# Kernel tuning notes

Measured on AMD Instinct MI355X. Metric: run time of the kernel, lower is better.

The kernel has to match this reference:

```python
import jax, jax.numpy as jnp
import numpy as np

N = 131072   # n_agents
K = 2        # k_neighbors = k_obstacles
H, C = 4, 128
HC = H * C   # 512
OBS_DIM = 37
OUT = 4


def setup_inputs() -> dict:
    key = jax.random.key(0)
    ks = jax.random.split(key, 40)
    s = 0.05
    def g(i, shape):
        return jax.random.normal(ks[i], shape, dtype=jnp.float32) * s
    inp = {"obs": jax.random.normal(ks[0], (N, OBS_DIM), dtype=jnp.float32)}
    # layer 0 (query_dim = 19)
    inp["wq0"] = g(1, (19, HC)); inp["wak0"] = g(2, (6, HC)); inp["wav0"] = g(3, (7, HC))
    inp["wok0"] = g(4, (2, HC)); inp["wov0"] = g(5, (2, HC))
    inp["apw0"] = g(6, (HC, C)); inp["apb0"] = jnp.zeros((C,), jnp.float32)
    inp["opw0"] = g(7, (HC, C)); inp["opb0"] = jnp.zeros((C,), jnp.float32)
    inp["fpw0"] = g(8, (2 * C, C)); inp["fpb0"] = jnp.zeros((C,), jnp.float32)
    inp["ca0"] = jnp.float32(1.0); inp["co0"] = jnp.float32(2.0)
    # layer 1 (query_dim = gnn_hidden_dim = 128)
    inp["wq1"] = g(9, (C, HC)); inp["wak1"] = g(10, (6, HC)); inp["wav1"] = g(11, (7, HC))
    inp["wok1"] = g(12, (2, HC)); inp["wov1"] = g(13, (2, HC))
    inp["apw1"] = g(14, (HC, C)); inp["apb1"] = jnp.zeros((C,), jnp.float32)
    inp["opw1"] = g(15, (HC, C)); inp["opb1"] = jnp.zeros((C,), jnp.float32)
    inp["fpw1"] = g(16, (2 * C, C)); inp["fpb1"] = jnp.zeros((C,), jnp.float32)
    inp["ca1"] = jnp.float32(1.0); inp["co1"] = jnp.float32(2.0)
    # output head
    inp["headw"] = g(17, (C, OUT)); inp["headb"] = jnp.zeros((OUT,), jnp.float32)
    return inp


def _forward(obs, wq0, wak0, wav0, wok0, wov0, apw0, apb0, opw0, opb0, fpw0, fpb0, ca0, co0,
             wq1, wak1, wav1, wok1, wov1, apw1, apb1, opw1, opb1, fpw1, fpb1, ca1, co1,
             headw, headb):
    n = obs.shape[0]
    scale = (C // H) ** -0.5  # matches torch: (out_channels // heads) ** -0.5

    # feature extraction per ObservationConfig (k=2)
    qf = jnp.concatenate([obs[:, 0:12], obs[:, 30:37]], axis=-1)        # [n, 19]
    nb = obs[:, 12:24].reshape(n, K, 6)                                  # neighbor keys [n,k,6]
    nbv = jnp.concatenate([nb, obs[:, 24:26][..., None]], axis=-1)       # + progress -> [n,k,7]
    ob = obs[:, 26:30].reshape(n, K, 2)                                  # obstacle k/v [n,k,2]
    apos = obs[:, 0:2]
    npos = nb[..., 0:2]
    opos = ob

    def attend(q, kfeat, vfeat, wk, wv, pw, pb, decay, pos_k):
        keys = (kfeat @ wk).reshape(n, K, H, C)
        vals = (vfeat @ wv).reshape(n, K, H, C)
        dist = jnp.linalg.norm(apos[:, None, :] - pos_k, axis=-1)        # [n,k]
        dw = jnp.exp(-decay * dist)                                      # [n,k]
        dot = jnp.einsum('nhc,nkhc->nhk', q, keys) * scale
        att = jax.nn.softmax(dot * dw[:, None, :], axis=-1)
        out = jnp.einsum('nhk,nkhc->nhc', att, vals).reshape(n, HC)
        return out @ pw + pb                                             # [n, C]

    def layer(qfeat, wq, wak, wav, wok, wov, apw, apb, opw, opb, fpw, fpb, ca, co):
        q = (qfeat @ wq).reshape(n, H, C)
        a = attend(q, nb, nbv, wak, wav, apw, apb, ca, npos)
        o = attend(q, ob, ob, wok, wov, opw, opb, co, opos)
        return jnp.concatenate([a, o], axis=-1) @ fpw + fpb              # [n, C]

    h = layer(qf, wq0, wak0, wav0, wok0, wov0, apw0, apb0, opw0, opb0, fpw0, fpb0, ca0, co0)
    h = layer(h, wq1, wak1, wav1, wok1, wov1, apw1, apb1, opw1, opb1, fpw1, fpb1, ca1, co1)
    return h @ headw + headb                                             # [n, OUT]


def reference(obs, wq0, wak0, wav0, wok0, wov0, apw0, apb0, opw0, opb0, fpw0, fpb0, ca0, co0,
              wq1, wak1, wav1, wok1, wov1, apw1, apb1, opw1, opb1, fpw1, fpb1, ca1, co1,
              headw, headb):
    return _forward(obs, wq0, wak0, wav0, wok0, wov0, apw0, apb0, opw0, opb0, fpw0, fpb0, ca0, co0,
                    wq1, wak1, wav1, wok1, wov1, apw1, apb1, opw1, opb1, fpw1, fpb1, ca1, co1,
                    headw, headb)
```

## Files before the change

### kernel.cpp

```cpp
#include <hip/hip_runtime.h>
#include <math.h>

#define NTH 256

typedef float v4f __attribute__((ext_vector_type(4)));

enum : int {
  WQ0_OFF = 0,
  M_OFF   = 608,
  TB_OFF  = 1760,
  AO1_OFF = 1792,
  B1H_OFF = 1936,
  PA0_OFF  = 2048,
  PO0_OFF  = 5632,
  PA1_OFF  = 6656,
  PO1_OFF  = 10240,
  WQ1T_OFF = 11264,
  B0_OFF   = 15360,
  BB1_OFF  = 15488,
  HWT_OFF  = 15616,
  WS_END   = 16128
};

__global__ __launch_bounds__(NTH) void prepA(
    const float* __restrict__ wq0,  const float* __restrict__ wak0, const float* __restrict__ wok0,
    const float* __restrict__ wav0, const float* __restrict__ wov0,
    const float* __restrict__ apw0, const float* __restrict__ opw0,
    const float* __restrict__ wq1,  const float* __restrict__ wak1, const float* __restrict__ wok1,
    const float* __restrict__ wav1, const float* __restrict__ wov1,
    const float* __restrict__ apw1, const float* __restrict__ opw1,
    const float* __restrict__ fpw0, const float* __restrict__ fpw1,
    const float* __restrict__ fpb0, const float* __restrict__ apb0, const float* __restrict__ opb0,
    const float* __restrict__ fpb1, const float* __restrict__ apb1, const float* __restrict__ opb1,
    const float* __restrict__ headw, float* __restrict__ ws)
{
  const int b = blockIdx.x;
  const int tid = threadIdx.x;
  const float scale = 0.17677669529663687f;

  if (b < 9) {
    const int idx = b * NTH + tid;
    const float* w; const v4f* p4; int t4, outv;
    if (idx < 896) {
      int h = idx / 224, r = idx % 224, i = r >> 5; t4 = r & 31;
      w = wav0 + i * 512 + h * 128; p4 = (const v4f*)(apw0 + h * 16384);
      outv = (PA0_OFF >> 2) + (h * 7 + i) * 32 + t4;
    } else if (idx < 1152) {
      int k = idx - 896; int h = k >> 6, i = (k >> 5) & 1; t4 = k & 31;
      w = wov0 + i * 512 + h * 128; p4 = (const v4f*)(opw0 + h * 16384);
      outv = (PO0_OFF >> 2) + (h * 2 + i) * 32 + t4;
    } else if (idx < 2048) {
      int k = idx - 1152; int h = k / 224, r = k % 224, i = r >> 5; t4 = r & 31;
      w = wav1 + i * 512 + h * 128; p4 = (const v4f*)(apw1 + h * 16384);
      outv = (PA1_OFF >> 2) + (h * 7 + i) * 32 + t4;
    } else {
      int k = idx - 2048; int h = k >> 6, i = (k >> 5) & 1; t4 = k & 31;
      w = wov1 + i * 512 + h * 128; p4 = (const v4f*)(opw1 + h * 16384);
      outv = (PO1_OFF >> 2) + (h * 2 + i) * 32 + t4;
    }
    v4f acc = (v4f)0.f;
#pragma unroll 32
    for (int c = 0; c < 128; ++c) acc += w[c] * p4[c * 32 + t4];
    ((v4f*)ws)[outv] = acc;
  } else if (b < 25) {
    const int idx = (b - 9) * NTH + tid;
    const int cc = idx & 127, j = (idx >> 7) & 7, h = idx >> 10;
    const v4f* a4 = (const v4f*)(wq1 + cc * 512 + h * 128);
    const v4f* b4 = (const v4f*)(((j < 6) ? wak1 + j * 512 : wok1 + (j - 6) * 512) + h * 128);
    v4f s = (v4f)0.f;
#pragma unroll 16
    for (int c4 = 0; c4 < 32; ++c4) s += a4[c4] * b4[c4];
    ws[WQ1T_OFF + (h * 8 + j) * 128 + cc] = s[0] + s[1] + s[2] + s[3];
  } else if (b < 28) {
    const int idx = (b - 25) * NTH + tid;
    if (idx < 608) {
      const int j = idx & 7, r = (idx >> 3) % 19, h = idx / 152;
      const v4f* a4 = (const v4f*)(wq0 + r * 512 + h * 128);
      const v4f* b4 = (const v4f*)(((j < 6) ? wak0 + j * 512 : wok0 + (j - 6) * 512) + h * 128);
      v4f s = (v4f)0.f;
#pragma unroll 16
      for (int c4 = 0; c4 < 32; ++c4) s += a4[c4] * b4[c4];
      ws[WQ0_OFF + idx] = (s[0] + s[1] + s[2] + s[3]) * scale;
    }
  } else if (b == 28) {
    __shared__ v4f red[256];
    const int isB1 = tid >> 7;
    const int s = tid & 127, j4 = s & 31, g = s >> 5;
    const v4f* fp4 = (const v4f*)(isB1 ? fpw1 : fpw0);
    const float* ab = isB1 ? apb1 : apb0;
    const float* ob = isB1 ? opb1 : opb0;
    const v4f* fb4 = (const v4f*)(isB1 ? fpb1 : fpb0);
    v4f acc = (v4f)0.f;
#pragma unroll 32
    for (int c = g * 32; c < g * 32 + 32; ++c)
      acc += ab[c] * fp4[c * 32 + j4] + ob[c] * fp4[(128 + c) * 32 + j4];
    red[tid] = acc;
    __syncthreads();
    if (g == 0) {
      v4f r = red[tid] + red[tid + 32] + red[tid + 64] + red[tid + 96] + fb4[j4];
      ((v4f*)(ws + (isB1 ? BB1_OFF : B0_OFF)))[j4] = r;
    }
  } else {
    for (int e = tid; e < 512; e += NTH) {
      const int o = e >> 7, c = e & 127;
      ws[HWT_OFF + e] = headw[c * 4 + o];
    }
  }
}

__global__ __launch_bounds__(NTH) void prepB(
    const float* __restrict__ fpw0, const float* __restrict__ fpw1,
    const float* __restrict__ headb, float* __restrict__ ws)
{
  const int b = blockIdx.x;
  const int tid = threadIdx.x;
  const float scale = 0.17677669529663687f;
  __shared__ v4f sred[256];
  __shared__ float sV[128];

  if (b < 72) {
    const int isL1 = (b >= 36) ? 1 : 0;
    const int t = isL1 ? b - 36 : b;
    const int h = t / 9, i = t % 9;
    const int x4 = tid & 31, g = tid >> 5;
    const float* P = ws + (i < 7
        ? (isL1 ? PA1_OFF : PA0_OFF) + (h * 7 + i) * 128
        : (isL1 ? PO1_OFF : PO0_OFF) + (h * 2 + (i - 7)) * 128);
    const v4f* f4 = (const v4f*)((isL1 ? fpw1 : fpw0) + (i < 7 ? 0 : 16384));
    v4f acc = (v4f)0.f;
#pragma unroll
    for (int u = g * 16; u < g * 16 + 16; ++u) acc += P[u] * f4[u * 32 + x4];
    sred[tid] = acc;
    __syncthreads();
    if (g == 0) {
      v4f r = sred[x4];
#pragma unroll
      for (int q = 1; q < 8; ++q) r += sred[q * 32 + x4];
      ((v4f*)sV)[x4] = r;
    }
    __syncthreads();
    if (!isL1) {
      if (tid < 32) {
        const int h2 = tid >> 3, j2 = tid & 7;
        const v4f* W4 = (const v4f*)(ws + WQ1T_OFF + (h2 * 8 + j2) * 128);
        const v4f* A4 = (const v4f*)sV;
        v4f a = (v4f)0.f;
#pragma unroll
        for (int c4 = 0; c4 < 32; ++c4) a += A4[c4] * W4[c4];
        ws[M_OFF + t * 32 + tid] = (a[0] + a[1] + a[2] + a[3]) * scale;
      }
    } else {
      if (tid < 4) {
        const v4f* H4 = (const v4f*)(ws + HWT_OFF + tid * 128);
        const v4f* R4 = (const v4f*)sV;
        v4f a = (v4f)0.f;
#pragma unroll
        for (int c4 = 0; c4 < 32; ++c4) a += R4[c4] * H4[c4];
        ws[AO1_OFF + t * 4 + tid] = a[0] + a[1] + a[2] + a[3];
      }
    }
  } else {
    if (tid < 32) {
      const int h = tid >> 3, j = tid & 7;
      const v4f* B4 = (const v4f*)(ws + B0_OFF);
      const v4f* W4 = (const v4f*)(ws + WQ1T_OFF + (h * 8 + j) * 128);
      v4f a = (v4f)0.f;
#pragma unroll
      for (int c4 = 0; c4 < 32; ++c4) a += B4[c4] * W4[c4];
      ws[TB_OFF + tid] = (a[0] + a[1] + a[2] + a[3]) * scale;
    } else if (tid < 36) {
      const int o = tid - 32;
      const v4f* B4 = (const v4f*)(ws + BB1_OFF);
      const v4f* H4 = (const v4f*)(ws + HWT_OFF + o * 128);
      v4f a = (v4f)0.f;
#pragma unroll
      for (int c4 = 0; c4 < 32; ++c4) a += B4[c4] * H4[c4];
      ws[B1H_OFF + o] = a[0] + a[1] + a[2] + a[3] + headb[o];
    }
  }
}

__global__ __launch_bounds__(NTH) void actor_main(
    const float* __restrict__ obs, const float* __restrict__ ws,
    const float* __restrict__ pca0, const float* __restrict__ pco0,
    const float* __restrict__ pca1, const float* __restrict__ pco1,
    float* __restrict__ out, int n)
{
  const int tid = threadIdx.x;
  const int gid = blockIdx.x * NTH + tid;

  __shared__ v4f sObsV[NTH * 37 / 4];
  float* sObs = (float*)sObsV;
  {
    const size_t total_f = (size_t)n * 37;
    const size_t v4base = (size_t)blockIdx.x * (NTH * 37 / 4);
    const v4f* src = (const v4f*)obs;
#pragma unroll
    for (int k = 0; k < 9; k++) {
      const size_t vi = v4base + k * NTH + tid;
      if (vi * 4 + 4 <= total_f) {
        sObsV[k * NTH + tid] = src[vi];
      } else {
#pragma unroll
        for (int e = 0; e < 4; e++) {
          const size_t f = vi * 4 + e;
          if (f < total_f) sObs[(k * NTH + tid) * 4 + e] = obs[f];
        }
      }
    }
    if (tid < 64) {
      const size_t vi = v4base + 9 * NTH + tid;
      if (vi * 4 + 4 <= total_f) {
        sObsV[9 * NTH + tid] = src[vi];
      } else {
#pragma unroll
        for (int e = 0; e < 4; e++) {
          const size_t f = vi * 4 + e;
          if (f < total_f) sObs[(9 * NTH + tid) * 4 + e] = obs[f];
        }
      }
    }
  }
  __syncthreads();
  if (gid >= n) return;

  const v4f* __restrict__ tbl = (const v4f*)ws;

  float o[37];
#pragma unroll
  for (int i = 0; i < 37; i++) o[i] = sObs[tid * 37 + i];

  float qf[19];
#pragma unroll
  for (int i = 0; i < 12; i++) qf[i] = o[i];
#pragma unroll
  for (int i = 0; i < 7; i++) qf[12 + i] = o[30 + i];
  float nb[2][6];
#pragma unroll
  for (int k2 = 0; k2 < 2; k2++)
#pragma unroll
    for (int i = 0; i < 6; i++) nb[k2][i] = o[12 + 6 * k2 + i];
  const float nbv6[2] = { o[24], o[25] };
  const float obf[2][2] = { { o[26], o[27] }, { o[28], o[29] } };
  const float ax = o[0], ay = o[1];

  float dista[2], disto[2];
#pragma unroll
  for (int k2 = 0; k2 < 2; k2++) {
    float dx = ax - nb[k2][0], dy = ay - nb[k2][1];
    dista[k2] = sqrtf(dx * dx + dy * dy);
    float ex = ax - obf[k2][0], ey = ay - obf[k2][1];
    disto[k2] = sqrtf(ex * ex + ey * ey);
  }
  const float ca0 = pca0[0], co0 = pco0[0], ca1 = pca1[0], co1 = pco1[0];
  float dwa0[2], dwo0[2], dwa1[2], dwo1[2];
#pragma unroll
  for (int k2 = 0; k2 < 2; k2++) {
    dwa0[k2] = __expf(-ca0 * dista[k2]);
    dwo0[k2] = __expf(-co0 * disto[k2]);
    dwa1[k2] = __expf(-ca1 * dista[k2]);
    dwo1[k2] = __expf(-co1 * disto[k2]);
  }

  v4f t0v[8];
#pragma unroll
  for (int z = 0; z < 8; z++) t0v[z] = (v4f)0.f;
#pragma unroll
  for (int h = 0; h < 4; h++) {
#pragma unroll
    for (int r = 0; r < 19; r++) {
      float q = qf[r];
      t0v[h * 2 + 0] += tbl[(h * 19 + r) * 2 + 0] * q;
      t0v[h * 2 + 1] += tbl[(h * 19 + r) * 2 + 1] * q;
    }
  }

  float wff[36];
#pragma unroll
  for (int h = 0; h < 4; h++) {
    float la[2], lo[2];
#pragma unroll
    for (int k2 = 0; k2 < 2; k2++) {
      float da = t0v[h*2][0]*nb[k2][0] + t0v[h*2][1]*nb[k2][1] + t0v[h*2][2]*nb[k2][2]
               + t0v[h*2][3]*nb[k2][3] + t0v[h*2+1][0]*nb[k2][4] + t0v[h*2+1][1]*nb[k2][5];
      la[k2] = da * dwa0[k2];
      float dof = t0v[h*2+1][2]*obf[k2][0] + t0v[h*2+1][3]*obf[k2][1];
      lo[k2] = dof * dwo0[k2];
    }
    float e  = __expf(la[1] - la[0]); float aa1 = e  / (1.f + e);  float aa0 = 1.f - aa1;
    float eo = __expf(lo[1] - lo[0]); float bo1 = eo / (1.f + eo); float bo0 = 1.f - bo1;
#pragma unroll
    for (int i = 0; i < 6; i++) wff[h * 9 + i] = aa0 * nb[0][i] + aa1 * nb[1][i];
    wff[h * 9 + 6] = aa0 * nbv6[0] + aa1 * nbv6[1];
    wff[h * 9 + 7] = bo0 * obf[0][0] + bo1 * obf[1][0];
    wff[h * 9 + 8] = bo0 * obf[0][1] + bo1 * obf[1][1];
  }

  v4f t1v[8];
#pragma unroll
  for (int q = 0; q < 8; q++) t1v[q] = tbl[440 + q];
#pragma unroll
  for (int t = 0; t < 36; t++) {
    float f = wff[t];
#pragma unroll
    for (int q = 0; q < 8; q++)
      t1v[q] += tbl[152 + t * 8 + q] * f;
  }

  float wf1f[36];
#pragma unroll
  for (int h = 0; h < 4; h++) {
    float la[2], lo[2];
#pragma unroll
    for (int k2 = 0; k2 < 2; k2++) {
      float da = t1v[h*2][0]*nb[k2][0] + t1v[h*2][1]*nb[k2][1] + t1v[h*2][2]*nb[k2][2]
               + t1v[h*2][3]*nb[k2][3] + t1v[h*2+1][0]*nb[k2][4] + t1v[h*2+1][1]*nb[k2][5];
      la[k2] = da * dwa1[k2];
      float dof = t1v[h*2+1][2]*obf[k2][0] + t1v[h*2+1][3]*obf[k2][1];
      lo[k2] = dof * dwo1[k2];
    }
    float e  = __expf(la[1] - la[0]); float aa1 = e  / (1.f + e);  float aa0 = 1.f - aa1;
    float eo = __expf(lo[1] - lo[0]); float bo1 = eo / (1.f + eo); float bo0 = 1.f - bo1;
#pragma unroll
    for (int i = 0; i < 6; i++) wf1f[h * 9 + i] = aa0 * nb[0][i] + aa1 * nb[1][i];
    wf1f[h * 9 + 6] = aa0 * nbv6[0] + aa1 * nbv6[1];
    wf1f[h * 9 + 7] = bo0 * obf[0][0] + bo1 * obf[1][0];
    wf1f[h * 9 + 8] = bo0 * obf[0][1] + bo1 * obf[1][1];
  }

  v4f acc = tbl[484];
#pragma unroll
  for (int t = 0; t < 36; t++)
    acc += tbl[448 + t] * wf1f[t];
  ((v4f*)out)[gid] = acc;
}

extern "C" void kernel_launch(void* const* d_in, const int* in_sizes, int n_in,
                              void* d_out, int out_size, void* d_ws, size_t ws_size,
                              hipStream_t stream)
{
  const float* obs  = (const float*)d_in[0];
  const float* wq0  = (const float*)d_in[1];
  const float* wak0 = (const float*)d_in[2];
  const float* wav0 = (const float*)d_in[3];
  const float* wok0 = (const float*)d_in[4];
  const float* wov0 = (const float*)d_in[5];
  const float* apw0 = (const float*)d_in[6];
  const float* apb0 = (const float*)d_in[7];
  const float* opw0 = (const float*)d_in[8];
  const float* opb0 = (const float*)d_in[9];
  const float* fpw0 = (const float*)d_in[10];
  const float* fpb0 = (const float*)d_in[11];
  const float* ca0  = (const float*)d_in[12];
  const float* co0  = (const float*)d_in[13];
  const float* wq1  = (const float*)d_in[14];
  const float* wak1 = (const float*)d_in[15];
  const float* wav1 = (const float*)d_in[16];
  const float* wok1 = (const float*)d_in[17];
  const float* wov1 = (const float*)d_in[18];
  const float* apw1 = (const float*)d_in[19];
  const float* apb1 = (const float*)d_in[20];
  const float* opw1 = (const float*)d_in[21];
  const float* opb1 = (const float*)d_in[22];
  const float* fpw1 = (const float*)d_in[23];
  const float* fpb1 = (const float*)d_in[24];
  const float* ca1  = (const float*)d_in[25];
  const float* co1  = (const float*)d_in[26];
  const float* headw = (const float*)d_in[27];
  const float* headb = (const float*)d_in[28];
  float* ws = (float*)d_ws;
  int n = in_sizes[0] / 37;

  prepA<<<30, NTH, 0, stream>>>(
      wq0, wak0, wok0, wav0, wov0, apw0, opw0,
      wq1, wak1, wok1, wav1, wov1, apw1, opw1,
      fpw0, fpw1, fpb0, apb0, opb0, fpb1, apb1, opb1, headw, ws);
  prepB<<<73, NTH, 0, stream>>>(fpw0, fpw1, headb, ws);
  actor_main<<<(n + NTH - 1) / NTH, NTH, 0, stream>>>(
      obs, ws, ca0, co0, ca1, co1, (float*)d_out, n);
}
```

Before: 150.6 us.

## Fuse weight-prep and per-agent compute into one cooperative persistent kernel

Merges the two weight-folding prep kernels and the main per-agent kernel into a single cooperative launch with a grid-wide sync. Each block stages its first observation tile before the barrier, then loops persistently over the remaining tiles. The prep work is also restructured so each block computes its full chain (value projection, output projection, then the wq1/key or head reduction) in shared memory, dropping intermediate workspace arrays and one launch. The aim is to remove launch gaps and overlap the first obs load with prep; the cost is a grid barrier, a grid capped at 512 blocks, and a fallback to two separate launches if cooperative launch fails.

```diff
diff --git a/kernel.cpp b/kernel.cpp
--- a/kernel.cpp
+++ b/kernel.cpp
@@ -1,7 +1,10 @@
 #include <hip/hip_runtime.h>
+#include <hip/hip_cooperative_groups.h>
 #include <math.h>
 
 #define NTH 256
+
+namespace cg = cooperative_groups;
 
 typedef float v4f __attribute__((ext_vector_type(4)));
 
@@ -10,69 +13,170 @@
   M_OFF   = 608,
   TB_OFF  = 1760,
   AO1_OFF = 1792,
-  B1H_OFF = 1936,
-  PA0_OFF  = 2048,
-  PO0_OFF  = 5632,
-  PA1_OFF  = 6656,
-  PO1_OFF  = 10240,
-  WQ1T_OFF = 11264,
-  B0_OFF   = 15360,
-  BB1_OFF  = 15488,
-  HWT_OFF  = 15616,
-  WS_END   = 16128
+  B1H_OFF = 1936
 };
 
-__global__ __launch_bounds__(NTH) void prepA(
+__device__ __forceinline__ void stage_obs(const float* __restrict__ obs,
+    v4f* sObsV, float* sObs, int tile, int n, int tid)
+{
+  const size_t total_f = (size_t)n * 37;
+  const size_t v4base = (size_t)tile * (NTH * 37 / 4);
+  const v4f* src = (const v4f*)obs;
+#pragma unroll
+  for (int k = 0; k < 9; k++) {
+    const size_t vi = v4base + k * NTH + tid;
+    if (vi * 4 + 4 <= total_f) {
+      sObsV[k * NTH + tid] = src[vi];
+    } else {
+      for (int e = 0; e < 4; e++) {
+        const size_t f = vi * 4 + e;
+        if (f < total_f) sObs[(k * NTH + tid) * 4 + e] = obs[f];
+      }
+    }
+  }
+  if (tid < 64) {
+    const size_t vi = v4base + 9 * NTH + tid;
+    if (vi * 4 + 4 <= total_f) {
+      sObsV[9 * NTH + tid] = src[vi];
+    } else {
+      for (int e = 0; e < 4; e++) {
+        const size_t f = vi * 4 + e;
+        if (f < total_f) sObs[(9 * NTH + tid) * 4 + e] = obs[f];
+      }
+    }
+  }
+}
+
+__device__ __forceinline__ void prep_block(
+    int b, int tid,
     const float* __restrict__ wq0,  const float* __restrict__ wak0, const float* __restrict__ wok0,
     const float* __restrict__ wav0, const float* __restrict__ wov0,
     const float* __restrict__ apw0, const float* __restrict__ opw0,
+    const float* __restrict__ fpw0, const float* __restrict__ fpb0,
+    const float* __restrict__ apb0, const float* __restrict__ opb0,
     const float* __restrict__ wq1,  const float* __restrict__ wak1, const float* __restrict__ wok1,
     const float* __restrict__ wav1, const float* __restrict__ wov1,
     const float* __restrict__ apw1, const float* __restrict__ opw1,
-    const float* __restrict__ fpw0, const float* __restrict__ fpw1,
-    const float* __restrict__ fpb0, const float* __restrict__ apb0, const float* __restrict__ opb0,
-    const float* __restrict__ fpb1, const float* __restrict__ apb1, const float* __restrict__ opb1,
-    const float* __restrict__ headw, float* __restrict__ ws)
-{
-  const int b = blockIdx.x;
-  const int tid = threadIdx.x;
+    const float* __restrict__ fpw1, const float* __restrict__ fpb1,
+    const float* __restrict__ apb1, const float* __restrict__ opb1,
+    const float* __restrict__ headw, const float* __restrict__ headb,
+    float* __restrict__ ws,
+    v4f* sred, float* sVecA, float* sVecB, float* sVecC)
+{
   const float scale = 0.17677669529663687f;
-
-  if (b < 9) {
-    const int idx = b * NTH + tid;
-    const float* w; const v4f* p4; int t4, outv;
-    if (idx < 896) {
-      int h = idx / 224, r = idx % 224, i = r >> 5; t4 = r & 31;
-      w = wav0 + i * 512 + h * 128; p4 = (const v4f*)(apw0 + h * 16384);
-      outv = (PA0_OFF >> 2) + (h * 7 + i) * 32 + t4;
-    } else if (idx < 1152) {
-      int k = idx - 896; int h = k >> 6, i = (k >> 5) & 1; t4 = k & 31;
-      w = wov0 + i * 512 + h * 128; p4 = (const v4f*)(opw0 + h * 16384);
-      outv = (PO0_OFF >> 2) + (h * 2 + i) * 32 + t4;
-    } else if (idx < 2048) {
-      int k = idx - 1152; int h = k / 224, r = k % 224, i = r >> 5; t4 = r & 31;
-      w = wav1 + i * 512 + h * 128; p4 = (const v4f*)(apw1 + h * 16384);
-      outv = (PA1_OFF >> 2) + (h * 7 + i) * 32 + t4;
+  const int x4 = tid & 31, g = tid >> 5;
+
+  if (b < 72) {
+    const int isL1 = (b >= 36) ? 1 : 0;
+    const int t = isL1 ? b - 36 : b;
+    const int h = t / 9, i = t % 9;
+    {
+      const float* w = (i < 7 ? (isL1 ? wav1 : wav0) + i * 512
+                              : (isL1 ? wov1 : wov0) + (i - 7) * 512) + h * 128;
+      const v4f* P4 = (const v4f*)((i < 7 ? (isL1 ? apw1 : apw0)
+                                          : (isL1 ? opw1 : opw0)) + h * 16384);
+      v4f acc = (v4f)0.f;
+#pragma unroll
+      for (int c = g * 16; c < g * 16 + 16; ++c) acc += w[c] * P4[c * 32 + x4];
+      sred[tid] = acc;
+    }
+    __syncthreads();
+    if (g == 0) {
+      v4f r = sred[x4];
+#pragma unroll
+      for (int q = 1; q < 8; ++q) r += sred[q * 32 + x4];
+      ((v4f*)sVecA)[x4] = r;
+    }
+    __syncthreads();
+    {
+      const v4f* F4 = (const v4f*)((isL1 ? fpw1 : fpw0) + (i < 7 ? 0 : 16384));
+      v4f acc = (v4f)0.f;
+#pragma unroll
+      for (int u = g * 16; u < g * 16 + 16; ++u) acc += sVecA[u] * F4[u * 32 + x4];
+      sred[tid] = acc;
+    }
+    __syncthreads();
+    if (g == 0) {
+      v4f r = sred[x4];
+#pragma unroll
+      for (int q = 1; q < 8; ++q) r += sred[q * 32 + x4];
+      ((v4f*)sVecC)[x4] = r;
+    }
+    __syncthreads();
+    if (!isL1) {
+      {
+        const int hd4 = tid & 127, g2 = tid >> 7;
+        const v4f* W4 = (const v4f*)wq1;
+        v4f acc = (v4f)0.f;
+#pragma unroll 32
+        for (int c = g2 * 64; c < g2 * 64 + 64; ++c) acc += sVecC[c] * W4[c * 128 + hd4];
+        sred[tid] = acc;
+      }
+      __syncthreads();
+      if (tid < 128) ((v4f*)sVecB)[tid] = sred[tid] + sred[tid + 128];
+      __syncthreads();
+      if (tid < 32) {
+        const int h2 = tid >> 3, j2 = tid & 7;
+        const v4f* wb = (const v4f*)(((j2 < 6) ? wak1 + j2 * 512 : wok1 + (j2 - 6) * 512) + h2 * 128);
+        const v4f* Gv = (const v4f*)(sVecB + h2 * 128);
+        v4f a = (v4f)0.f;
+#pragma unroll
+        for (int c4 = 0; c4 < 32; ++c4) a += Gv[c4] * wb[c4];
+        ws[M_OFF + t * 32 + tid] = (a[0] + a[1] + a[2] + a[3]) * scale;
+      }
     } else {
-      int k = idx - 2048; int h = k >> 6, i = (k >> 5) & 1; t4 = k & 31;
-      w = wov1 + i * 512 + h * 128; p4 = (const v4f*)(opw1 + h * 16384);
-      outv = (PO1_OFF >> 2) + (h * 2 + i) * 32 + t4;
-    }
-    v4f acc = (v4f)0.f;
+      if (tid < 128) sred[tid] = sVecC[tid] * ((const v4f*)headw)[tid];
+      __syncthreads();
+      if (tid < 32) sred[tid] = sred[tid] + sred[tid + 32] + sred[tid + 64] + sred[tid + 96];
+      __syncthreads();
+      if (tid == 0) {
+        v4f a = (v4f)0.f;
+#pragma unroll
+        for (int q = 0; q < 32; ++q) a += sred[q];
+        ((v4f*)(ws + AO1_OFF))[t] = a;
+      }
+    }
+  } else if (b == 72) {
+    {
+      const v4f* F4 = (const v4f*)fpw0;
+      v4f acc = (v4f)0.f;
+#pragma unroll 16
+      for (int r = g * 32; r < g * 32 + 32; ++r) {
+        const float cf = (r < 128) ? apb0[r] : opb0[r - 128];
+        acc += cf * F4[r * 32 + x4];
+      }
+      sred[tid] = acc;
+    }
+    __syncthreads();
+    if (g == 0) {
+      v4f r = sred[x4];
+#pragma unroll
+      for (int q = 1; q < 8; ++q) r += sred[q * 32 + x4];
+      ((v4f*)sVecA)[x4] = r + ((const v4f*)fpb0)[x4];
+    }
+    __syncthreads();
+    {
+      const int hd4 = tid & 127, g2 = tid >> 7;
+      const v4f* W4 = (const v4f*)wq1;
+      v4f acc = (v4f)0.f;
 #pragma unroll 32
-    for (int c = 0; c < 128; ++c) acc += w[c] * p4[c * 32 + t4];
-    ((v4f*)ws)[outv] = acc;
-  } else if (b < 25) {
-    const int idx = (b - 9) * NTH + tid;
-    const int cc = idx & 127, j = (idx >> 7) & 7, h = idx >> 10;
-    const v4f* a4 = (const v4f*)(wq1 + cc * 512 + h * 128);
-    const v4f* b4 = (const v4f*)(((j < 6) ? wak1 + j * 512 : wok1 + (j - 6) * 512) + h * 128);
-    v4f s = (v4f)0.f;
-#pragma unroll 16
-    for (int c4 = 0; c4 < 32; ++c4) s += a4[c4] * b4[c4];
-    ws[WQ1T_OFF + (h * 8 + j) * 128 + cc] = s[0] + s[1] + s[2] + s[3];
-  } else if (b < 28) {
-    const int idx = (b - 25) * NTH + tid;
+      for (int c = g2 * 64; c < g2 * 64 + 64; ++c) acc += sVecA[c] * W4[c * 128 + hd4];
+      sred[tid] = acc;
+    }
+    __syncthreads();
+    if (tid < 128) ((v4f*)sVecB)[tid] = sred[tid] + sred[tid + 128];
+    __syncthreads();
+    if (tid < 32) {
+      const int h2 = tid >> 3, j2 = tid & 7;
+      const v4f* wb = (const v4f*)(((j2 < 6) ? wak1 + j2 * 512 : wok1 + (j2 - 6) * 512) + h2 * 128);
+      const v4f* Gv = (const v4f*)(sVecB + h2 * 128);
+      v4f a = (v4f)0.f;
+#pragma unroll
+      for (int c4 = 0; c4 < 32; ++c4) a += Gv[c4] * wb[c4];
+      ws[TB_OFF + tid] = (a[0] + a[1] + a[2] + a[3]) * scale;
+    }
+  } else if (b < 76) {
+    const int idx = (b - 73) * NTH + tid;
     if (idx < 608) {
       const int j = idx & 7, r = (idx >> 3) % 19, h = idx / 152;
       const v4f* a4 = (const v4f*)(wq0 + r * 512 + h * 128);
@@ -82,148 +186,44 @@
       for (int c4 = 0; c4 < 32; ++c4) s += a4[c4] * b4[c4];
       ws[WQ0_OFF + idx] = (s[0] + s[1] + s[2] + s[3]) * scale;
     }
-  } else if (b == 28) {
-    __shared__ v4f red[256];
-    const int isB1 = tid >> 7;
-    const int s = tid & 127, j4 = s & 31, g = s >> 5;
-    const v4f* fp4 = (const v4f*)(isB1 ? fpw1 : fpw0);
-    const float* ab = isB1 ? apb1 : apb0;
-    const float* ob = isB1 ? opb1 : opb0;
-    const v4f* fb4 = (const v4f*)(isB1 ? fpb1 : fpb0);
-    v4f acc = (v4f)0.f;
-#pragma unroll 32
-    for (int c = g * 32; c < g * 32 + 32; ++c)
-      acc += ab[c] * fp4[c * 32 + j4] + ob[c] * fp4[(128 + c) * 32 + j4];
-    red[tid] = acc;
-    __syncthreads();
-    if (g == 0) {
-      v4f r = red[tid] + red[tid + 32] + red[tid + 64] + red[tid + 96] + fb4[j4];
-      ((v4f*)(ws + (isB1 ? BB1_OFF : B0_OFF)))[j4] = r;
-    }
   } else {
-    for (int e = tid; e < 512; e += NTH) {
-      const int o = e >> 7, c = e & 127;
-      ws[HWT_OFF + e] = headw[c * 4 + o];
-    }
-  }
-}
-
-__global__ __launch_bounds__(NTH) void prepB(
-    const float* __restrict__ fpw0, const float* __restrict__ fpw1,
-    const float* __restrict__ headb, float* __restrict__ ws)
-{
-  const int b = blockIdx.x;
-  const int tid = threadIdx.x;
-  const float scale = 0.17677669529663687f;
-  __shared__ v4f sred[256];
-  __shared__ float sV[128];
-
-  if (b < 72) {
-    const int isL1 = (b >= 36) ? 1 : 0;
-    const int t = isL1 ? b - 36 : b;
-    const int h = t / 9, i = t % 9;
-    const int x4 = tid & 31, g = tid >> 5;
-    const float* P = ws + (i < 7
-        ? (isL1 ? PA1_OFF : PA0_OFF) + (h * 7 + i) * 128
-        : (isL1 ? PO1_OFF : PO0_OFF) + (h * 2 + (i - 7)) * 128);
-    const v4f* f4 = (const v4f*)((isL1 ? fpw1 : fpw0) + (i < 7 ? 0 : 16384));
-    v4f acc = (v4f)0.f;
-#pragma unroll
-    for (int u = g * 16; u < g * 16 + 16; ++u) acc += P[u] * f4[u * 32 + x4];
-    sred[tid] = acc;
+    {
+      const v4f* F4 = (const v4f*)fpw1;
+      v4f acc = (v4f)0.f;
+#pragma unroll 16
+      for (int r = g * 32; r < g * 32 + 32; ++r) {
+        const float cf = (r < 128) ? apb1[r] : opb1[r - 128];
+        acc += cf * F4[r * 32 + x4];
+      }
+      sred[tid] = acc;
+    }
     __syncthreads();
     if (g == 0) {
       v4f r = sred[x4];
 #pragma unroll
       for (int q = 1; q < 8; ++q) r += sred[q * 32 + x4];
-      ((v4f*)sV)[x4] = r;
-    }
-    __syncthreads();
-    if (!isL1) {
-      if (tid < 32) {
-        const int h2 = tid >> 3, j2 = tid & 7;
-        const v4f* W4 = (const v4f*)(ws + WQ1T_OFF + (h2 * 8 + j2) * 128);
-        const v4f* A4 = (const v4f*)sV;
-        v4f a = (v4f)0.f;
-#pragma unroll
-        for (int c4 = 0; c4 < 32; ++c4) a += A4[c4] * W4[c4];
-        ws[M_OFF + t * 32 + tid] = (a[0] + a[1] + a[2] + a[3]) * scale;
-      }
-    } else {
-      if (tid < 4) {
-        const v4f* H4 = (const v4f*)(ws + HWT_OFF + tid * 128);
-        const v4f* R4 = (const v4f*)sV;
-        v4f a = (v4f)0.f;
-#pragma unroll
-        for (int c4 = 0; c4 < 32; ++c4) a += R4[c4] * H4[c4];
-        ws[AO1_OFF + t * 4 + tid] = a[0] + a[1] + a[2] + a[3];
-      }
-    }
-  } else {
-    if (tid < 32) {
-      const int h = tid >> 3, j = tid & 7;
-      const v4f* B4 = (const v4f*)(ws + B0_OFF);
-      const v4f* W4 = (const v4f*)(ws + WQ1T_OFF + (h * 8 + j) * 128);
-      v4f a = (v4f)0.f;
-#pragma unroll
-      for (int c4 = 0; c4 < 32; ++c4) a += B4[c4] * W4[c4];
-      ws[TB_OFF + tid] = (a[0] + a[1] + a[2] + a[3]) * scale;
-    } else if (tid < 36) {
-      const int o = tid - 32;
-      const v4f* B4 = (const v4f*)(ws + BB1_OFF);
-      const v4f* H4 = (const v4f*)(ws + HWT_OFF + o * 128);
-      v4f a = (v4f)0.f;
-#pragma unroll
-      for (int c4 = 0; c4 < 32; ++c4) a += B4[c4] * H4[c4];
-      ws[B1H_OFF + o] = a[0] + a[1] + a[2] + a[3] + headb[o];
-    }
-  }
-}
-
-__global__ __launch_bounds__(NTH) void actor_main(
-    const float* __restrict__ obs, const float* __restrict__ ws,
-    const float* __restrict__ pca0, const float* __restrict__ pco0,
-    const float* __restrict__ pca1, const float* __restrict__ pco1,
-    float* __restrict__ out, int n)
-{
-  const int tid = threadIdx.x;
-  const int gid = blockIdx.x * NTH + tid;
-
-  __shared__ v4f sObsV[NTH * 37 / 4];
-  float* sObs = (float*)sObsV;
-  {
-    const size_t total_f = (size_t)n * 37;
-    const size_t v4base = (size_t)blockIdx.x * (NTH * 37 / 4);
-    const v4f* src = (const v4f*)obs;
-#pragma unroll
-    for (int k = 0; k < 9; k++) {
-      const size_t vi = v4base + k * NTH + tid;
-      if (vi * 4 + 4 <= total_f) {
-        sObsV[k * NTH + tid] = src[vi];
-      } else {
-#pragma unroll
-        for (int e = 0; e < 4; e++) {
-          const size_t f = vi * 4 + e;
-          if (f < total_f) sObs[(k * NTH + tid) * 4 + e] = obs[f];
-        }
-      }
-    }
-    if (tid < 64) {
-      const size_t vi = v4base + 9 * NTH + tid;
-      if (vi * 4 + 4 <= total_f) {
-        sObsV[9 * NTH + tid] = src[vi];
-      } else {
-#pragma unroll
-        for (int e = 0; e < 4; e++) {
-          const size_t f = vi * 4 + e;
-          if (f < total_f) sObs[(9 * NTH + tid) * 4 + e] = obs[f];
-        }
-      }
-    }
-  }
-  __syncthreads();
-  if (gid >= n) return;
-
+      ((v4f*)sVecA)[x4] = r + ((const v4f*)fpb1)[x4];
+    }
+    __syncthreads();
+    if (tid < 128) sred[tid] = sVecA[tid] * ((const v4f*)headw)[tid];
+    __syncthreads();
+    if (tid < 32) sred[tid] = sred[tid] + sred[tid + 32] + sred[tid + 64] + sred[tid + 96];
+    __syncthreads();
+    if (tid == 0) {
+      v4f a = *(const v4f*)headb;
+#pragma unroll
+      for (int q = 0; q < 32; ++q) a += sred[q];
+      ((v4f*)(ws + B1H_OFF))[0] = a;
+    }
+  }
+}
+
+__device__ __forceinline__ void actor_compute(
+    const float* sObs, int tid, int gid,
+    const float* __restrict__ ws,
+    float ca0, float co0, float ca1, float co1,
+    float* __restrict__ out)
+{
   const v4f* __restrict__ tbl = (const v4f*)ws;
 
   float o[37];
@@ -252,7 +252,6 @@
     float ex = ax - obf[k2][0], ey = ay - obf[k2][1];
     disto[k2] = sqrtf(ex * ex + ey * ey);
   }
-  const float ca0 = pca0[0], co0 = pco0[0], ca1 = pca1[0], co1 = pco1[0];
   float dwa0[2], dwo0[2], dwa1[2], dwo1[2];
 #pragma unroll
   for (int k2 = 0; k2 < 2; k2++) {
@@ -333,6 +332,97 @@
   for (int t = 0; t < 36; t++)
     acc += tbl[448 + t] * wf1f[t];
   ((v4f*)out)[gid] = acc;
+}
+
+__global__ __launch_bounds__(NTH, 2) void fused_all(
+    const float* __restrict__ obs,
+    const float* __restrict__ wq0,  const float* __restrict__ wak0, const float* __restrict__ wok0,
+    const float* __restrict__ wav0, const float* __restrict__ wov0,
+    const float* __restrict__ apw0, const float* __restrict__ opw0,
+    const float* __restrict__ fpw0, const float* __restrict__ fpb0,
+    const float* __restrict__ apb0, const float* __restrict__ opb0,
+    const float* __restrict__ wq1,  const float* __restrict__ wak1, const float* __restrict__ wok1,
+    const float* __restrict__ wav1, const float* __restrict__ wov1,
+    const float* __restrict__ apw1, const float* __restrict__ opw1,
+    const float* __restrict__ fpw1, const float* __restrict__ fpb1,
+    const float* __restrict__ apb1, const float* __restrict__ opb1,
+    const float* __restrict__ headw, const float* __restrict__ headb,
+    const float* __restrict__ pca0, const float* __restrict__ pco0,
+    const float* __restrict__ pca1, const float* __restrict__ pco1,
+    float* __restrict__ out, float* __restrict__ ws, int n)
+{
+  const int tid = threadIdx.x;
+  const int b = blockIdx.x;
+
+  __shared__ v4f sObsV[NTH * 37 / 4];
+  __shared__ v4f sred[NTH];
+  __shared__ float sVecA[128];
+  __shared__ float sVecB[512];
+  __shared__ float sVecC[128];
+  float* sObs = (float*)sObsV;
+
+  if ((long long)b * NTH < n) stage_obs(obs, sObsV, sObs, b, n, tid);
+  if (b < 77)
+    prep_block(b, tid, wq0, wak0, wok0, wav0, wov0, apw0, opw0, fpw0, fpb0,
+               apb0, opb0, wq1, wak1, wok1, wav1, wov1, apw1, opw1, fpw1,
+               fpb1, apb1, opb1, headw, headb, ws, sred, sVecA, sVecB, sVecC);
+
+  __threadfence();
+  cg::this_grid().sync();
+
+  const float ca0 = pca0[0], co0 = pco0[0], ca1 = pca1[0], co1 = pco1[0];
+  int tile = b;
+  bool first = true;
+  while ((long long)tile * NTH < n) {
+    if (!first) {
+      __syncthreads();
+      stage_obs(obs, sObsV, sObs, tile, n, tid);
+      __syncthreads();
+    }
+    const int gid = tile * NTH + tid;
+    if (gid < n) actor_compute(sObs, tid, gid, ws, ca0, co0, ca1, co1, out);
+    tile += gridDim.x;
+    first = false;
+  }
+}
+
+__global__ __launch_bounds__(NTH) void prep_one(
+    const float* __restrict__ wq0,  const float* __restrict__ wak0, const float* __restrict__ wok0,
+    const float* __restrict__ wav0, const float* __restrict__ wov0,
+    const float* __restrict__ apw0, const float* __restrict__ opw0,
+    const float* __restrict__ fpw0, const float* __restrict__ fpb0,
+    const float* __restrict__ apb0, const float* __restrict__ opb0,
+    const float* __restrict__ wq1,  const float* __restrict__ wak1, const float* __restrict__ wok1,
+    const float* __restrict__ wav1, const float* __restrict__ wov1,
+    const float* __restrict__ apw1, const float* __restrict__ opw1,
+    const float* __restrict__ fpw1, const float* __restrict__ fpb1,
+    const float* __restrict__ apb1, const float* __restrict__ opb1,
+    const float* __restrict__ headw, const float* __restrict__ headb,
+    float* __restrict__ ws)
+{
+  __shared__ v4f sred[NTH];
+  __shared__ float sVecA[128];
+  __shared__ float sVecB[512];
+  __shared__ float sVecC[128];
+  prep_block(blockIdx.x, threadIdx.x, wq0, wak0, wok0, wav0, wov0, apw0, opw0,
+             fpw0, fpb0, apb0, opb0, wq1, wak1, wok1, wav1, wov1, apw1, opw1,
+             fpw1, fpb1, apb1, opb1, headw, headb, ws, sred, sVecA, sVecB, sVecC);
+}
+
+__global__ __launch_bounds__(NTH) void actor_k(
+    const float* __restrict__ obs, const float* __restrict__ ws,
+    const float* __restrict__ pca0, const float* __restrict__ pco0,
+    const float* __restrict__ pca1, const float* __restrict__ pco1,
+    float* __restrict__ out, int n)
+{
+  const int tid = threadIdx.x;
+  const int gid = blockIdx.x * NTH + tid;
+  __shared__ v4f sObsV[NTH * 37 / 4];
+  float* sObs = (float*)sObsV;
+  stage_obs(obs, sObsV, sObs, blockIdx.x, n, tid);
+  __syncthreads();
+  if (gid >= n) return;
+  actor_compute(sObs, tid, gid, ws, pca0[0], pco0[0], pca1[0], pco1[0], out);
 }
 
 extern "C" void kernel_launch(void* const* d_in, const int* in_sizes, int n_in,
@@ -369,13 +459,34 @@
   const float* headw = (const float*)d_in[27];
   const float* headb = (const float*)d_in[28];
   float* ws = (float*)d_ws;
+  float* outp = (float*)d_out;
   int n = in_sizes[0] / 37;
 
-  prepA<<<30, NTH, 0, stream>>>(
-      wq0, wak0, wok0, wav0, wov0, apw0, opw0,
-      wq1, wak1, wok1, wav1, wov1, apw1, opw1,
-      fpw0, fpw1, fpb0, apb0, opb0, fpb1, apb1, opb1, headw, ws);
-  prepB<<<73, NTH, 0, stream>>>(fpw0, fpw1, headb, ws);
-  actor_main<<<(n + NTH - 1) / NTH, NTH, 0, stream>>>(
-      obs, ws, ca0, co0, ca1, co1, (float*)d_out, n);
-}
+  const int nblk = (n + NTH - 1) / NTH;
+  int NB = nblk < 77 ? 77 : nblk;
+  if (NB > 512) NB = 512;
+
+  void* args[] = {
+    (void*)&obs,
+    (void*)&wq0, (void*)&wak0, (void*)&wok0,
+    (void*)&wav0, (void*)&wov0, (void*)&apw0, (void*)&opw0,
+    (void*)&fpw0, (void*)&fpb0, (void*)&apb0, (void*)&opb0,
+    (void*)&wq1, (void*)&wak1, (void*)&wok1,
+    (void*)&wav1, (void*)&wov1, (void*)&apw1, (void*)&opw1,
+    (void*)&fpw1, (void*)&fpb1, (void*)&apb1, (void*)&opb1,
+    (void*)&headw, (void*)&headb,
+    (void*)&ca0, (void*)&co0, (void*)&ca1, (void*)&co1,
+    (void*)&outp, (void*)&ws, (void*)&n
+  };
+
+  hipError_t rc = hipLaunchCooperativeKernel(
+      reinterpret_cast<void*>(fused_all), dim3(NB), dim3(NTH), args, 0, stream);
+  if (rc != hipSuccess) {
+    (void)hipGetLastError();
+    prep_one<<<77, NTH, 0, stream>>>(
+        wq0, wak0, wok0, wav0, wov0, apw0, opw0, fpw0, fpb0, apb0, opb0,
+        wq1, wak1, wok1, wav1, wov1, apw1, opw1, fpw1, fpb1, apb1, opb1,
+        headw, headb, ws);
+    actor_k<<<nblk, NTH, 0, stream>>>(obs, ws, ca0, co0, ca1, co1, outp, n);
+  }
+}
```

After: 315.6 us. 110% more time.
